# Performance work log

Hardware: AMD Instinct MI355X
Metric: run time of the kernel (lower is better)

## Reference

```python
import jax, jax.numpy as jnp
import numpy as np

D_IN = 1024
D_OUT = 1024
N = 4096


def setup_inputs() -> dict:
    key = jax.random.key(0)
    kx, kq, kk, kv = jax.random.split(key, 4)
    x = jax.random.normal(kx, (N, D_IN), dtype=jnp.float32)
    # weights stored as [d_in, d_out] so that x @ W == torch Linear(x)
    s = 1.0 / np.sqrt(D_IN)
    W_q = jax.random.uniform(kq, (D_IN, D_OUT), jnp.float32, -s, s)
    W_k = jax.random.uniform(kk, (D_IN, D_OUT), jnp.float32, -s, s)
    W_v = jax.random.uniform(kv, (D_IN, D_OUT), jnp.float32, -s, s)
    return {"x": x, "W_q": W_q, "W_k": W_k, "W_v": W_v}


def reference(x, W_q, W_k, W_v):
    # x: [N, d_in]; projections -> [N, d_out]
    q = x @ W_q
    k = x @ W_k
    v = x @ W_v
    scale = 1.0 / jnp.sqrt(jnp.asarray(k.shape[-1], dtype=q.dtype))
    scores = (q @ k.T) * scale            # [N, N]
    weights = jax.nn.softmax(scores, axis=-1)
    return weights @ v                     # [N, d_out]
```

## Files before the change

### kernel.cpp

```cpp
#include <hip/hip_runtime.h>
#include <math.h>

typedef _Float16 f16;
typedef __attribute__((ext_vector_type(8))) _Float16 f16x8;
typedef __attribute__((ext_vector_type(4))) _Float16 f16x4;
typedef __attribute__((ext_vector_type(4))) float f32x4;

#define NSEQ 4096
#define DIN 1024
#define DOUT 1024

__device__ __forceinline__ void load16(const void* g, void* l) {
    __builtin_amdgcn_global_load_lds(
        (const __attribute__((address_space(1))) unsigned int*)g,
        (__attribute__((address_space(3))) unsigned int*)l, 16, 0, 0);
}

template <typename OutT, int EPI>
__global__ __launch_bounds__(256, 2)
void gemm_bt(const f16* __restrict__ A, const f16* __restrict__ B,
             OutT* __restrict__ c0, OutT* __restrict__ c1,
             OutT* __restrict__ c2, OutT* __restrict__ c3,
             int M, int N, int K, int lda, int ldb, int ldc, float scale,
             long aStrideZ, long bStrideZ,
             f16* __restrict__ TC, int tz, int ldt, float* __restrict__ Sums)
{
    const int z = blockIdx.z;
    A += (long)z * aStrideZ;
    B += (long)z * bStrideZ;
    OutT* C = z == 0 ? c0 : (z == 1 ? c1 : (z == 2 ? c2 : c3));
    __shared__ f16 As[2 * 128 * 32];
    __shared__ f16 Bs[2 * 128 * 32];

    int gx = gridDim.x;
    int bid = blockIdx.y * gx + blockIdx.x;
    int xcd = bid & 7, s = bid >> 3;
    int px = s & 7, rest = s >> 3;
    int py = rest & 3, chunk = rest >> 2;
    int pg = xcd + (chunk << 3);
    int pcols = gx >> 3;
    int lp = 31 - __clz(pcols);
    int bx = ((pg & (pcols - 1)) << 3) + px;
    int by = ((pg >> lp) << 2) + py;

    const int t    = threadIdx.x;
    const int lane = t & 63;
    const int wave = t >> 6;
    const int wm   = (wave >> 1) * 64;
    const int wn   = (wave & 1) * 64;
    const int tile_m = by * 128;
    const int tile_n = bx * 128;
    const int quad = lane >> 4;
    const int l16  = lane & 15;
    const int srow = t >> 2;
    const int scol = ((t & 3) ^ (srow & 3)) * 8;
    const int qx8 = (quad ^ (l16 & 3)) * 8;

    f32x4 acc[4][4];
#pragma unroll
    for (int i = 0; i < 4; i++)
#pragma unroll
        for (int j = 0; j < 4; j++)
            acc[i][j] = (f32x4){0.f, 0.f, 0.f, 0.f};

    const f16* Ab = A + (long)(tile_m + srow) * lda + scol;
    const f16* Bb = B + (long)(tile_n + srow) * ldb + scol;
    f16* Asd = As + t * 8;
    f16* Bsd = Bs + t * 8;

    for (int k0 = 0; k0 < K; k0 += 64) {
        load16(Ab + k0, Asd);
        load16(Ab + (long)64 * lda + k0, Asd + 2048);
        load16(Ab + k0 + 32, Asd + 4096);
        load16(Ab + (long)64 * lda + k0 + 32, Asd + 4096 + 2048);
        load16(Bb + k0, Bsd);
        load16(Bb + (long)64 * ldb + k0, Bsd + 2048);
        load16(Bb + k0 + 32, Bsd + 4096);
        load16(Bb + (long)64 * ldb + k0 + 32, Bsd + 4096 + 2048);
        __syncthreads();
#pragma unroll
        for (int p = 0; p < 2; p++) {
            f16x8 a[4], b[4];
#pragma unroll
            for (int i = 0; i < 4; i++)
                a[i] = *(const f16x8*)(As + p * 4096 + (wm + i * 16 + l16) * 32 + qx8);
#pragma unroll
            for (int j = 0; j < 4; j++)
                b[j] = *(const f16x8*)(Bs + p * 4096 + (wn + j * 16 + l16) * 32 + qx8);
#pragma unroll
            for (int i = 0; i < 4; i++)
#pragma unroll
                for (int j = 0; j < 4; j++)
                    acc[i][j] = __builtin_amdgcn_mfma_f32_16x16x32_f16(
                        a[i], b[j], acc[i][j], 0, 0, 0);
        }
        __syncthreads();
    }
    if (EPI == 1) {
        if (z == tz) {
#pragma unroll
            for (int i = 0; i < 4; i++)
#pragma unroll
                for (int j = 0; j < 4; j++) {
                    f16x4 o;
#pragma unroll
                    for (int r = 0; r < 4; r++) o[r] = (f16)(acc[i][j][r] * scale);
                    int row0 = tile_m + wm + i * 16 + quad * 4;
                    int col  = tile_n + wn + j * 16 + l16;
                    *(f16x4*)(TC + (long)col * ldt + row0) = o;
                }
        } else {
#pragma unroll
            for (int i = 0; i < 4; i++)
#pragma unroll
                for (int j = 0; j < 4; j++)
#pragma unroll
                    for (int r = 0; r < 4; r++) {
                        int row = tile_m + wm + i * 16 + quad * 4 + r;
                        int col = tile_n + wn + j * 16 + l16;
                        C[(long)row * ldc + col] = (OutT)(acc[i][j][r] * scale);
                    }
        }
    } else if (EPI == 2) {
        const int bxs = bx * 2 + (wn >> 6);
#pragma unroll
        for (int i = 0; i < 4; i++) {
            float rs[4] = {0.f, 0.f, 0.f, 0.f};
#pragma unroll
            for (int j = 0; j < 4; j++)
#pragma unroll
                for (int r = 0; r < 4; r++) {
                    float e = __expf(acc[i][j][r] * scale);
                    int row = tile_m + wm + i * 16 + quad * 4 + r;
                    int col = tile_n + wn + j * 16 + l16;
                    C[(long)row * ldc + col] = (OutT)e;
                    rs[r] += e;
                }
#pragma unroll
            for (int msk = 1; msk < 16; msk <<= 1)
#pragma unroll
                for (int r = 0; r < 4; r++)
                    rs[r] += __shfl_xor(rs[r], msk, 64);
            if (l16 == 0)
#pragma unroll
                for (int r = 0; r < 4; r++) {
                    int row = tile_m + wm + i * 16 + quad * 4 + r;
                    Sums[(long)row * 64 + bxs] = rs[r];
                }
        }
    } else {
#pragma unroll
        for (int i = 0; i < 4; i++)
#pragma unroll
            for (int j = 0; j < 4; j++)
#pragma unroll
                for (int r = 0; r < 4; r++) {
                    int row = tile_m + wm + i * 16 + quad * 4 + r;
                    int col = tile_n + wn + j * 16 + l16;
                    C[(long)row * ldc + col] = (OutT)(acc[i][j][r] * scale);
                }
    }
}

__global__ void prep(const float* __restrict__ x,
                     const float* __restrict__ W0, const float* __restrict__ W1,
                     const float* __restrict__ W2,
                     f16* __restrict__ xb, f16* __restrict__ Wt) {
    if (blockIdx.z == 3) {
        long base = ((long)(blockIdx.y * 16 + blockIdx.x) * 256 + threadIdx.x) * 4;
#pragma unroll
        for (int it = 0; it < 16; it++) {
            long i = base + (long)it * (256 * 256 * 4);
            f32x4 v = *(const f32x4*)(x + i);
            f16x4 o;
            o.x = (f16)v.x; o.y = (f16)v.y; o.z = (f16)v.z; o.w = (f16)v.w;
            *(f16x4*)(xb + i) = o;
        }
        return;
    }
    __shared__ f16 tile[64][65];
    const float* W = blockIdx.z == 0 ? W0 : (blockIdx.z == 1 ? W1 : W2);
    f16* O = Wt + (long)blockIdx.z * DIN * DOUT;
    int r0 = blockIdx.y * 64;
    int c0 = blockIdx.x * 64;
    int tx = threadIdx.x & 63, ty = threadIdx.x >> 6;
#pragma unroll
    for (int i = 0; i < 16; i++)
        tile[ty + i * 4][tx] = (f16)W[(long)(r0 + ty + i * 4) * DOUT + c0 + tx];
    __syncthreads();
#pragma unroll
    for (int i = 0; i < 16; i++)
        O[(long)(c0 + ty + i * 4) * DIN + r0 + tx] = tile[tx][ty + i * 4];
}

__global__ __launch_bounds__(256)
void reduce_norm(const f16* __restrict__ p0, const f16* __restrict__ p1,
                 const f16* __restrict__ p2, const f16* __restrict__ p3,
                 const float* __restrict__ sums, float* __restrict__ out) {
    const int row = blockIdx.x;
    const int lane = threadIdx.x & 63;
    float s = sums[(long)row * 64 + lane];
#pragma unroll
    for (int msk = 1; msk < 64; msk <<= 1) s += __shfl_xor(s, msk, 64);
    const float inv = 1.f / s;
    long i = (long)row * 1024 + threadIdx.x * 4;
    f16x4 a = *(const f16x4*)(p0 + i);
    f16x4 b = *(const f16x4*)(p1 + i);
    f16x4 c = *(const f16x4*)(p2 + i);
    f16x4 d = *(const f16x4*)(p3 + i);
    f32x4 o;
    o.x = (((float)a.x + (float)b.x) + ((float)c.x + (float)d.x)) * inv;
    o.y = (((float)a.y + (float)b.y) + ((float)c.y + (float)d.y)) * inv;
    o.z = (((float)a.z + (float)b.z) + ((float)c.z + (float)d.z)) * inv;
    o.w = (((float)a.w + (float)b.w) + ((float)c.w + (float)d.w)) * inv;
    *(f32x4*)(out + i) = o;
}

extern "C" void kernel_launch(void* const* d_in, const int* in_sizes, int n_in,
                              void* d_out, int out_size, void* d_ws, size_t ws_size,
                              hipStream_t stream) {
    const float* x  = (const float*)d_in[0];
    const float* Wq = (const float*)d_in[1];
    const float* Wk = (const float*)d_in[2];
    const float* Wv = (const float*)d_in[3];
    float* out = (float*)d_out;
    char* ws = (char*)d_ws;
    const size_t MB = 1ull << 20;
    f16* xb  = (f16*)(ws);
    f16* Wt  = (f16*)(ws + 8 * MB);
    f16* Qb  = (f16*)(ws + 14 * MB);
    f16* Kb  = (f16*)(ws + 22 * MB);
    f16* Vt  = (f16*)(ws + 30 * MB);
    f16* S   = (f16*)(ws + 38 * MB);
    f16* scr0 = (f16*)(ws + 70 * MB);
    f16* scr1 = (f16*)(ws + 78 * MB);
    f16* scr2 = (f16*)(ws + 86 * MB);
    f16* scr3 = (f16*)(ws + 94 * MB);
    float* Sums = (float*)(ws);

    prep<<<dim3(16, 16, 4), 256, 0, stream>>>(x, Wq, Wk, Wv, xb, Wt);
    gemm_bt<f16, 1><<<dim3(8, 32, 3), 256, 0, stream>>>(
        xb, Wt, Qb, Kb, Qb, Qb, NSEQ, DOUT, DIN, DIN, DIN, DOUT, 1.0f,
        0, (long)DIN * DOUT, Vt, 2, NSEQ, nullptr);
    gemm_bt<f16, 2><<<dim3(32, 32, 1), 256, 0, stream>>>(
        Qb, Kb, S, S, S, S, NSEQ, NSEQ, DIN, DIN, DIN, NSEQ, 0.03125f,
        0, 0, nullptr, -1, 0, Sums);
    gemm_bt<f16, 0><<<dim3(8, 32, 4), 256, 0, stream>>>(
        S, Vt, scr0, scr1, scr2, scr3, NSEQ, DOUT, 1024, NSEQ, NSEQ, DOUT, 1.0f,
        1024, 1024, nullptr, -1, 0, nullptr);
    reduce_norm<<<4096, 256, 0, stream>>>(scr0, scr1, scr2, scr3, Sums, out);
}
```

Before: 199.9 us.

## Rewrite GEMM as 256x256 tile, 8-wave, double-buffered pipelined kernel

New measurement: 223.4 us. +11.8%, slower.

```diff
diff --git a/kernel.cpp b/kernel.cpp
--- a/kernel.cpp
+++ b/kernel.cpp
@@ -16,8 +16,22 @@
         (__attribute__((address_space(3))) unsigned int*)l, 16, 0, 0);
 }
 
+#define MEMFENCE asm volatile("" ::: "memory")
+#define BAR() do { MEMFENCE; __builtin_amdgcn_s_barrier(); MEMFENCE; } while (0)
+
+#define MM(I, J, KH, AR) \
+    acc[I][J] = __builtin_amdgcn_mfma_f32_16x16x32_f16(AR[KH], b##J[KH], acc[I][J], 0, 0, 0)
+
+#define MFMA16(I0, I1) \
+    __builtin_amdgcn_s_setprio(1); \
+    MM(I0,0,0,a0); MM(I0,1,0,a0); MM(I0,2,0,a0); MM(I0,3,0,a0); \
+    MM(I1,0,0,a1); MM(I1,1,0,a1); MM(I1,2,0,a1); MM(I1,3,0,a1); \
+    MM(I0,0,1,a0); MM(I0,1,1,a0); MM(I0,2,1,a0); MM(I0,3,1,a0); \
+    MM(I1,0,1,a1); MM(I1,1,1,a1); MM(I1,2,1,a1); MM(I1,3,1,a1); \
+    __builtin_amdgcn_s_setprio(0)
+
 template <typename OutT, int EPI>
-__global__ __launch_bounds__(256, 2)
+__global__ __launch_bounds__(512, 2)
 void gemm_bt(const f16* __restrict__ A, const f16* __restrict__ B,
              OutT* __restrict__ c0, OutT* __restrict__ c1,
              OutT* __restrict__ c2, OutT* __restrict__ c3,
@@ -29,77 +43,106 @@
     A += (long)z * aStrideZ;
     B += (long)z * bStrideZ;
     OutT* C = z == 0 ? c0 : (z == 1 ? c1 : (z == 2 ? c2 : c3));
-    __shared__ f16 As[2 * 128 * 32];
-    __shared__ f16 Bs[2 * 128 * 32];
-
-    int gx = gridDim.x;
-    int bid = blockIdx.y * gx + blockIdx.x;
-    int xcd = bid & 7, s = bid >> 3;
-    int px = s & 7, rest = s >> 3;
-    int py = rest & 3, chunk = rest >> 2;
-    int pg = xcd + (chunk << 3);
-    int pcols = gx >> 3;
-    int lp = 31 - __clz(pcols);
-    int bx = ((pg & (pcols - 1)) << 3) + px;
-    int by = ((pg >> lp) << 2) + py;
-
-    const int t    = threadIdx.x;
-    const int lane = t & 63;
-    const int wave = t >> 6;
-    const int wm   = (wave >> 1) * 64;
-    const int wn   = (wave & 1) * 64;
-    const int tile_m = by * 128;
-    const int tile_n = bx * 128;
+    __shared__ f16 As[2 * 256 * 64];
+    __shared__ f16 Bs[2 * 256 * 64];
+
+    const int gx = gridDim.x;
+    const int nwg = gx * gridDim.y;
+    const int bid0 = blockIdx.y * gx + blockIdx.x;
+    const int nb = (bid0 & 7) * (nwg >> 3) + (bid0 >> 3);
+    const int bx = nb % gx, by = nb / gx;
+
+    const int tid  = threadIdx.x;
+    const int lane = tid & 63;
+    const int w    = tid >> 6;
+    const int wm   = (w >> 2) * 128;
+    const int wn   = (w & 3) * 64;
+    const int tile_m = by * 256;
+    const int tile_n = bx * 256;
     const int quad = lane >> 4;
     const int l16  = lane & 15;
-    const int srow = t >> 2;
-    const int scol = ((t & 3) ^ (srow & 3)) * 8;
-    const int qx8 = (quad ^ (l16 & 3)) * 8;
-
-    f32x4 acc[4][4];
-#pragma unroll
-    for (int i = 0; i < 4; i++)
-#pragma unroll
-        for (int j = 0; j < 4; j++)
-            acc[i][j] = (f32x4){0.f, 0.f, 0.f, 0.f};
-
-    const f16* Ab = A + (long)(tile_m + srow) * lda + scol;
-    const f16* Bb = B + (long)(tile_n + srow) * ldb + scol;
-    f16* Asd = As + t * 8;
-    f16* Bsd = Bs + t * 8;
-
-    for (int k0 = 0; k0 < K; k0 += 64) {
-        load16(Ab + k0, Asd);
-        load16(Ab + (long)64 * lda + k0, Asd + 2048);
-        load16(Ab + k0 + 32, Asd + 4096);
-        load16(Ab + (long)64 * lda + k0 + 32, Asd + 4096 + 2048);
-        load16(Bb + k0, Bsd);
-        load16(Bb + (long)64 * ldb + k0, Bsd + 2048);
-        load16(Bb + k0 + 32, Bsd + 4096);
-        load16(Bb + (long)64 * ldb + k0 + 32, Bsd + 4096 + 2048);
-        __syncthreads();
-#pragma unroll
-        for (int p = 0; p < 2; p++) {
-            f16x8 a[4], b[4];
-#pragma unroll
-            for (int i = 0; i < 4; i++)
-                a[i] = *(const f16x8*)(As + p * 4096 + (wm + i * 16 + l16) * 32 + qx8);
-#pragma unroll
-            for (int j = 0; j < 4; j++)
-                b[j] = *(const f16x8*)(Bs + p * 4096 + (wn + j * 16 + l16) * 32 + qx8);
-#pragma unroll
-            for (int i = 0; i < 4; i++)
-#pragma unroll
-                for (int j = 0; j < 4; j++)
-                    acc[i][j] = __builtin_amdgcn_mfma_f32_16x16x32_f16(
-                        a[i], b[j], acc[i][j], 0, 0, 0);
-        }
-        __syncthreads();
-    }
+
+    const f16* Ab = A + (long)(tile_m + (w >> 1) * 16 + l16) * lda + (w & 1) * 32 + quad * 8;
+    const f16* Bb = B + (long)(tile_n + (w >> 1) * 16 + l16) * ldb + (w & 1) * 32 + quad * 8;
+    const long a64 = (long)64 * lda, b64 = (long)64 * ldb;
+    char* ldsA = (char*)As + w * 1024;
+    char* ldsB = (char*)Bs + w * 1024;
+
+    auto stA = [&](int buf, int h, int L, int k0) {
+        load16(Ab + (long)(h * 2 + L) * a64 + k0, ldsA + buf * 32768 + h * 16384 + L * 8192);
+    };
+    auto stB = [&](int buf, int h, int L, int k0) {
+        load16(Bb + (long)(h * 2 + L) * b64 + k0, ldsB + buf * 32768 + h * 16384 + L * 8192);
+    };
+
+    const char* aRd = (const char*)As + (wm >> 7) * 16384 + lane * 16;
+    const char* bRd = (const char*)Bs + (wn >> 7) * 16384 + ((wn >> 6) & 1) * 8192 + lane * 16;
+
+    f32x4 acc[8][4];
+#pragma unroll
+    for (int i = 0; i < 8; i++)
+#pragma unroll
+        for (int j = 0; j < 4; j++) acc[i][j] = (f32x4){0.f, 0.f, 0.f, 0.f};
+
+    const int nt = K >> 6;
+
+    stA(0, 0, 0, 0); stA(0, 0, 1, 0); stA(0, 1, 0, 0); stA(0, 1, 1, 0);
+    stB(0, 0, 0, 0); stB(0, 0, 1, 0); stB(0, 1, 0, 0); stB(0, 1, 1, 0);
+    if (nt > 1) {
+        stB(1, 0, 0, 64); stB(1, 0, 1, 64); stB(1, 1, 0, 64); stB(1, 1, 1, 64);
+        asm volatile("s_waitcnt vmcnt(4)" ::: "memory");
+    } else {
+        asm volatile("s_waitcnt vmcnt(0)" ::: "memory");
+    }
+    BAR();
+
+    for (int ti = 0; ti < nt; ++ti) {
+        const int cur = ti & 1;
+        const char* aR = aRd + cur * 32768;
+        const char* bR = bRd + cur * 32768;
+        const int k1 = (ti + 1) << 6;
+        const int k2 = (ti + 2) << 6;
+        f16x8 b0[2], b1[2], b2[2], b3[2], a0[2], a1[2];
+        b0[0] = *(const f16x8*)(bR);          b0[1] = *(const f16x8*)(bR + 1024);
+        b1[0] = *(const f16x8*)(bR + 2048);   b1[1] = *(const f16x8*)(bR + 3072);
+        b2[0] = *(const f16x8*)(bR + 4096);   b2[1] = *(const f16x8*)(bR + 5120);
+        b3[0] = *(const f16x8*)(bR + 6144);   b3[1] = *(const f16x8*)(bR + 7168);
+        a0[0] = *(const f16x8*)(aR);          a0[1] = *(const f16x8*)(aR + 1024);
+        a1[0] = *(const f16x8*)(aR + 2048);   a1[1] = *(const f16x8*)(aR + 3072);
+        if (ti + 1 < nt) { stA(cur ^ 1, 0, 0, k1); stA(cur ^ 1, 0, 1, k1); }
+        BAR();
+        __builtin_amdgcn_sched_barrier(0);
+        MFMA16(0, 1);
+        BAR();
+        a0[0] = *(const f16x8*)(aR + 4096);   a0[1] = *(const f16x8*)(aR + 5120);
+        a1[0] = *(const f16x8*)(aR + 6144);   a1[1] = *(const f16x8*)(aR + 7168);
+        if (ti + 1 < nt) { stA(cur ^ 1, 1, 0, k1); stA(cur ^ 1, 1, 1, k1); }
+        BAR();
+        __builtin_amdgcn_sched_barrier(0);
+        MFMA16(2, 3);
+        BAR();
+        a0[0] = *(const f16x8*)(aR + 8192);   a0[1] = *(const f16x8*)(aR + 9216);
+        a1[0] = *(const f16x8*)(aR + 10240);  a1[1] = *(const f16x8*)(aR + 11264);
+        if (ti + 2 < nt) { stB(cur, 0, 0, k2); stB(cur, 0, 1, k2); }
+        BAR();
+        __builtin_amdgcn_sched_barrier(0);
+        MFMA16(4, 5);
+        BAR();
+        a0[0] = *(const f16x8*)(aR + 12288);  a0[1] = *(const f16x8*)(aR + 13312);
+        a1[0] = *(const f16x8*)(aR + 14336);  a1[1] = *(const f16x8*)(aR + 15360);
+        if (ti + 2 < nt) { stB(cur, 1, 0, k2); stB(cur, 1, 1, k2); }
+        BAR();
+        __builtin_amdgcn_sched_barrier(0);
+        MFMA16(6, 7);
+        if (ti + 2 < nt)      asm volatile("s_waitcnt vmcnt(4)" ::: "memory");
+        else if (ti + 1 < nt) asm volatile("s_waitcnt vmcnt(0)" ::: "memory");
+        BAR();
+    }
+
     if (EPI == 1) {
         if (z == tz) {
 #pragma unroll
-            for (int i = 0; i < 4; i++)
+            for (int i = 0; i < 8; i++)
 #pragma unroll
                 for (int j = 0; j < 4; j++) {
                     f16x4 o;
@@ -111,7 +154,7 @@
                 }
         } else {
 #pragma unroll
-            for (int i = 0; i < 4; i++)
+            for (int i = 0; i < 8; i++)
 #pragma unroll
                 for (int j = 0; j < 4; j++)
 #pragma unroll
@@ -122,9 +165,9 @@
                     }
         }
     } else if (EPI == 2) {
-        const int bxs = bx * 2 + (wn >> 6);
-#pragma unroll
-        for (int i = 0; i < 4; i++) {
+        const int bxs = bx * 4 + (wn >> 6);
+#pragma unroll
+        for (int i = 0; i < 8; i++) {
             float rs[4] = {0.f, 0.f, 0.f, 0.f};
 #pragma unroll
             for (int j = 0; j < 4; j++)
@@ -150,7 +193,7 @@
         }
     } else {
 #pragma unroll
-        for (int i = 0; i < 4; i++)
+        for (int i = 0; i < 8; i++)
 #pragma unroll
             for (int j = 0; j < 4; j++)
 #pragma unroll
@@ -239,13 +282,13 @@
     float* Sums = (float*)(ws);
 
     prep<<<dim3(16, 16, 4), 256, 0, stream>>>(x, Wq, Wk, Wv, xb, Wt);
-    gemm_bt<f16, 1><<<dim3(8, 32, 3), 256, 0, stream>>>(
+    gemm_bt<f16, 1><<<dim3(4, 16, 3), 512, 0, stream>>>(
         xb, Wt, Qb, Kb, Qb, Qb, NSEQ, DOUT, DIN, DIN, DIN, DOUT, 1.0f,
         0, (long)DIN * DOUT, Vt, 2, NSEQ, nullptr);
-    gemm_bt<f16, 2><<<dim3(32, 32, 1), 256, 0, stream>>>(
+    gemm_bt<f16, 2><<<dim3(16, 16, 1), 512, 0, stream>>>(
         Qb, Kb, S, S, S, S, NSEQ, NSEQ, DIN, DIN, DIN, NSEQ, 0.03125f,
         0, 0, nullptr, -1, 0, Sums);
-    gemm_bt<f16, 0><<<dim3(8, 32, 4), 256, 0, stream>>>(
+    gemm_bt<f16, 0><<<dim3(4, 16, 4), 512, 0, stream>>>(
         S, Vt, scr0, scr1, scr2, scr3, NSEQ, DOUT, 1024, NSEQ, NSEQ, DOUT, 1.0f,
         1024, 1024, nullptr, -1, 0, nullptr);
     reduce_norm<<<4096, 256, 0, stream>>>(scr0, scr1, scr2, scr3, Sums, out);
```
